# Kernel optimization log

Measured on AMD Instinct MI355X. Metric: run time of the kernel, lower is better.

The kernel has to match this reference:

```python
import jax, jax.numpy as jnp
import numpy as np

DIM = 1024
H = 16
HD = DIM // H
SCALE = HD ** -0.5
LAMBDA_INIT = 0.1
EPS = 1e-6


def setup_inputs() -> dict:
    key0 = jax.random.key(0)
    ks = jax.random.split(key0, 12)
    B, Nq, Nk = 2, 1024, 2048
    w = 0.02
    inp = {
        "query": jax.random.normal(ks[0], (B, Nq, DIM), jnp.float32),
        "key": jax.random.normal(ks[1], (B, Nk, DIM), jnp.float32),
        "value": jax.random.normal(ks[2], (B, Nk, DIM), jnp.float32),
        "qpos": jax.random.randint(ks[3], (B, Nq), 0, Nq, jnp.int32),
        "kpos": jax.random.randint(ks[4], (B, Nk), 0, Nk, jnp.int32),
        "q1_w": jax.random.normal(ks[5], (DIM, DIM), jnp.float32) * w,
        "q2_w": jax.random.normal(ks[6], (DIM, DIM), jnp.float32) * w,
        "kv1_w": jax.random.normal(ks[7], (2 * DIM, DIM), jnp.float32) * w,
        "kv2_w": jax.random.normal(ks[8], (2 * DIM, DIM), jnp.float32) * w,
        "proj_w": jax.random.normal(ks[9], (DIM, DIM), jnp.float32) * w,
        "proj_b": jnp.zeros((DIM,), jnp.float32),
        "norm_w": jnp.ones((DIM,), jnp.float32),
        "lambda_1": jnp.ones((1, H, 1, 1), jnp.float32),
        # layer_idx=0, max_layer=12 -> scale = 1/12
        "lambda_2": jnp.full((1, H, 1, 1), 1.0 - LAMBDA_INIT * (1.0 / 12.0), jnp.float32),
    }
    return inp


def _split_heads(x, B, N):
    # [B, N, DIM] -> [B, H, N, HD]
    return x.reshape(B, N, H, HD).transpose(0, 2, 1, 3)


def reference(query, key, value, qpos, kpos, q1_w, q2_w, kv1_w, kv2_w,
              proj_w, proj_b, norm_w, lambda_1, lambda_2):
    B, Nq, C = query.shape
    Nk = key.shape[1]

    q1 = _split_heads(query @ q1_w.T, B, Nq)
    q2 = _split_heads(query @ q2_w.T, B, Nq)

    kv1 = (key @ kv1_w.T).reshape(B, Nk, 2, H, HD).transpose(2, 0, 3, 1, 4)
    k1, v1 = kv1[0], kv1[1]  # [B, H, Nk, HD]
    kv2 = (key @ kv2_w.T).reshape(B, Nk, 2, H, HD).transpose(2, 0, 3, 1, 4)
    k2 = kv2[0]

    attn1 = jax.nn.softmax(jnp.einsum('bhqd,bhkd->bhqk', q1, k1) * SCALE, axis=-1)
    attn2 = jax.nn.softmax(jnp.einsum('bhqd,bhkd->bhqk', q2, k2) * SCALE, axis=-1)

    lambda_full = lambda_1 - lambda_2 + LAMBDA_INIT  # [1, H, 1, 1]
    diff_attn = attn1 - lambda_full * attn2

    x = jnp.einsum('bhqk,bhkd->bhqd', diff_attn, v1)
    x = x.transpose(0, 2, 1, 3).reshape(B, Nq, C)

    # RMSNorm (computed in float32 like the original)
    xf = x.astype(jnp.float32)
    xf = xf * jax.lax.rsqrt(jnp.mean(xf * xf, axis=-1, keepdims=True) + EPS) * norm_w
    x = xf.astype(x.dtype)

    return x @ proj_w.T + proj_b
```

## Files before the change

### kernel.cpp

```cpp
#include <hip/hip_runtime.h>
#include <cstdint>

typedef unsigned short u16;
typedef __bf16 bf16x8 __attribute__((ext_vector_type(8)));
typedef float f32x4 __attribute__((ext_vector_type(4)));

#define SCALE_LOG2E (0.125f * 1.44269504088896340736f)

__device__ __forceinline__ u16 f2bf(float f) {
    uint32_t u = __builtin_bit_cast(uint32_t, f);
    u += 0x7fff + ((u >> 16) & 1);
    return (u16)(u >> 16);
}
__device__ __forceinline__ float bf2f(u16 u) {
    return __builtin_bit_cast(float, (uint32_t)u << 16);
}

__device__ __forceinline__ void gload_lds16(const void* g, void* l) {
    __builtin_amdgcn_global_load_lds(
        (__attribute__((address_space(1))) void*)g,
        (__attribute__((address_space(3))) void*)l, 16, 0, 0);
}

__global__ __launch_bounds__(256) void cvt_all(const float* __restrict__ s0,
                                               const float* __restrict__ s1,
                                               const float* __restrict__ s2,
                                               const float* __restrict__ s3,
                                               const float* __restrict__ s4,
                                               const float* __restrict__ s5,
                                               const float* __restrict__ s6,
                                               u16* __restrict__ d0, u16* __restrict__ d1,
                                               u16* __restrict__ d2, u16* __restrict__ d3,
                                               u16* __restrict__ d4) {
    int i = blockIdx.x * 256 + threadIdx.x;
    const float* src;
    u16* dst;
    int off;
    if (i < 524288)       { src = s0; dst = d0; off = i; }
    else if (i < 1572864) { src = s1; dst = d1; off = i - 524288; }
    else if (i < 1835008) { src = s2; dst = d2; off = i - 1572864; }
    else if (i < 2097152) { src = s3; dst = d2 + (size_t)1024 * 1024; off = i - 1835008; }
    else if (i < 2621440) { src = s4; dst = d3; off = i - 2097152; }
    else if (i < 2883584) { src = s5; dst = d3 + (size_t)2048 * 1024; off = i - 2621440; }
    else                  { src = s6; dst = d4; off = i - 2883584; }
    float4 v = ((const float4*)src)[off];
    ushort4 o;
    o.x = f2bf(v.x); o.y = f2bf(v.y); o.z = f2bf(v.z); o.w = f2bf(v.w);
    ((ushort4*)dst)[off] = o;
}

__global__ __launch_bounds__(256) void gemm_qkv(const u16* __restrict__ Xq,
                                                const u16* __restrict__ Wq,
                                                const u16* __restrict__ Xk,
                                                const u16* __restrict__ Wkv,
                                                u16* __restrict__ q1s, u16* __restrict__ q2s,
                                                u16* __restrict__ k1s, u16* __restrict__ v1t,
                                                u16* __restrict__ k2s) {
    __shared__ u16 As[128 * 32];
    __shared__ u16 Bs[128 * 32];
    const int K = 1024;
    const int bid = blockIdx.x;
    int mode, bm, bn;
    const u16 *A, *B;
    if (bid < 256) {
        mode = 0; bm = bid >> 4; bn = bid & 15; A = Xq; B = Wq;
    } else {
        int t = bid - 256;
        mode = 1; bm = t / 24; bn = t % 24; A = Xk; B = Wkv;
    }
    const int tid = threadIdx.x;
    const int l = tid & 63, w = tid >> 6;
    const int c = l & 15, g = l >> 4;
    const int wr = w >> 1, wc = w & 1;

    f32x4 acc[4][4];
#pragma unroll
    for (int i = 0; i < 4; i++)
#pragma unroll
        for (int j = 0; j < 4; j++) acc[i][j] = f32x4{0.f, 0.f, 0.f, 0.f};

    const u16* Abase = A + (size_t)(bm * 128) * K;
    const u16* Bbase = B + (size_t)(bn * 128) * K;
    const int r0 = 32 * w + (l >> 2);
    const int ch = (l & 3) * 8;

    for (int kb = 0; kb < K; kb += 32) {
        gload_lds16(Abase + (size_t)r0 * K + kb + ch,        As + 32 * w * 32);
        gload_lds16(Abase + (size_t)(r0 + 16) * K + kb + ch, As + (32 * w + 16) * 32);
        gload_lds16(Bbase + (size_t)r0 * K + kb + ch,        Bs + 32 * w * 32);
        gload_lds16(Bbase + (size_t)(r0 + 16) * K + kb + ch, Bs + (32 * w + 16) * 32);
        __syncthreads();
        bf16x8 af[4], bfr[4];
#pragma unroll
        for (int mi = 0; mi < 4; mi++)
            af[mi] = *(const bf16x8*)&As[(64 * wr + 16 * mi + c) * 32 + 8 * g];
#pragma unroll
        for (int ni = 0; ni < 4; ni++)
            bfr[ni] = *(const bf16x8*)&Bs[(64 * wc + 16 * ni + c) * 32 + 8 * g];
#pragma unroll
        for (int mi = 0; mi < 4; mi++)
#pragma unroll
            for (int ni = 0; ni < 4; ni++)
                acc[mi][ni] = __builtin_amdgcn_mfma_f32_16x16x32_bf16(
                    af[mi], bfr[ni], acc[mi][ni], 0, 0, 0);
        __syncthreads();
    }

#pragma unroll
    for (int mi = 0; mi < 4; mi++)
#pragma unroll
        for (int ni = 0; ni < 4; ni++)
#pragma unroll
            for (int j = 0; j < 4; j++) {
                int m = bm * 128 + 64 * wr + 16 * mi + 4 * g + j;
                int n = bn * 128 + 64 * wc + 16 * ni + c;
                float v = acc[mi][ni][j];
                if (mode == 0) {
                    int b = m >> 10, nq = m & 1023;
                    int half = n >> 10, nn = n & 1023;
                    int h = nn >> 6, hd = nn & 63;
                    u16* dst = half ? q2s : q1s;
                    dst[(size_t)((b * 16 + h) * 1024 + nq) * 64 + hd] = f2bf(v * SCALE_LOG2E);
                } else {
                    int b = m >> 11, nk = m & 2047;
                    if (n < 1024) {
                        int h = n >> 6, hd = n & 63;
                        k1s[(size_t)((b * 16 + h) * 2048 + nk) * 64 + hd] = f2bf(v);
                    } else if (n < 2048) {
                        int nn = n - 1024, h = nn >> 6, hd = nn & 63;
                        v1t[(size_t)((b * 16 + h) * 64 + hd) * 2048 + nk] = f2bf(v);
                    } else {
                        int nn = n - 2048, h = nn >> 6, hd = nn & 63;
                        k2s[(size_t)((b * 16 + h) * 2048 + nk) * 64 + hd] = f2bf(v);
                    }
                }
            }
}

__global__ __launch_bounds__(256) void gemm_proj(const u16* __restrict__ A,
                                                 const u16* __restrict__ B,
                                                 float* __restrict__ fo,
                                                 const float* __restrict__ bias) {
    __shared__ u16 As[128 * 32];
    __shared__ u16 Bs[64 * 32];
    const int K = 1024;
    const int bm = blockIdx.x >> 4, bn = blockIdx.x & 15;
    const int tid = threadIdx.x;
    const int l = tid & 63, w = tid >> 6;
    const int c = l & 15, g = l >> 4;
    const int wr = w >> 1, wc = w & 1;

    f32x4 acc[4][2];
#pragma unroll
    for (int i = 0; i < 4; i++)
#pragma unroll
        for (int j = 0; j < 2; j++) acc[i][j] = f32x4{0.f, 0.f, 0.f, 0.f};

    const u16* Abase = A + (size_t)(bm * 128) * K;
    const u16* Bbase = B + (size_t)(bn * 64) * K;
    const int rA = 32 * w + (l >> 2);
    const int rB = 16 * w + (l >> 2);
    const int ch = (l & 3) * 8;

    for (int kb = 0; kb < K; kb += 32) {
        gload_lds16(Abase + (size_t)rA * K + kb + ch,        As + 32 * w * 32);
        gload_lds16(Abase + (size_t)(rA + 16) * K + kb + ch, As + (32 * w + 16) * 32);
        gload_lds16(Bbase + (size_t)rB * K + kb + ch,        Bs + 16 * w * 32);
        __syncthreads();
        bf16x8 af[4], bfr[2];
#pragma unroll
        for (int mi = 0; mi < 4; mi++)
            af[mi] = *(const bf16x8*)&As[(64 * wr + 16 * mi + c) * 32 + 8 * g];
#pragma unroll
        for (int ni = 0; ni < 2; ni++)
            bfr[ni] = *(const bf16x8*)&Bs[(32 * wc + 16 * ni + c) * 32 + 8 * g];
#pragma unroll
        for (int mi = 0; mi < 4; mi++)
#pragma unroll
            for (int ni = 0; ni < 2; ni++)
                acc[mi][ni] = __builtin_amdgcn_mfma_f32_16x16x32_bf16(
                    af[mi], bfr[ni], acc[mi][ni], 0, 0, 0);
        __syncthreads();
    }

#pragma unroll
    for (int mi = 0; mi < 4; mi++)
#pragma unroll
        for (int ni = 0; ni < 2; ni++)
#pragma unroll
            for (int j = 0; j < 4; j++) {
                int m = bm * 128 + 64 * wr + 16 * mi + 4 * g + j;
                int n = bn * 64 + 32 * wc + 16 * ni + c;
                fo[(size_t)m * 1024 + n] = acc[mi][ni][j] + bias[n];
            }
}

__global__ __launch_bounds__(256) void attn_kernel(const u16* __restrict__ q1s,
                                                   const u16* __restrict__ q2s,
                                                   const u16* __restrict__ k1s,
                                                   const u16* __restrict__ k2s,
                                                   const u16* __restrict__ v1t,
                                                   u16* __restrict__ Opart,
                                                   float* __restrict__ Lpart) {
    __shared__ __bf16 P1[4][32 * 72];
    __shared__ __bf16 P2[4][32 * 72];
    const int tid = threadIdx.x;
    const int l = tid & 63, w = tid >> 6;
    const int c = l & 15, g = l >> 4;
    const int bid = blockIdx.x;
    const int xcd = bid & 7, slot = bid >> 3;
    const int bh = xcd * 4 + (slot >> 5);
    const int r = slot & 31;
    const int qt = r >> 2, s = r & 3;
    const int b = bh >> 4, h = bh & 15;
    const int q0 = qt * 128 + w * 32;

    bf16x8 qf1[2][2], qf2[2][2];
#pragma unroll
    for (int qq = 0; qq < 2; qq++) {
        const u16* p1 = q1s + (size_t)(bh * 1024 + q0 + qq * 16 + c) * 64 + 8 * g;
        const u16* p2 = q2s + (size_t)(bh * 1024 + q0 + qq * 16 + c) * 64 + 8 * g;
        qf1[qq][0] = *(const bf16x8*)p1; qf1[qq][1] = *(const bf16x8*)(p1 + 32);
        qf2[qq][0] = *(const bf16x8*)p2; qf2[qq][1] = *(const bf16x8*)(p2 + 32);
    }

    f32x4 O1[2][4], O2[2][4], la1[2], la2[2];
#pragma unroll
    for (int qq = 0; qq < 2; qq++) {
        la1[qq] = la2[qq] = f32x4{0.f, 0.f, 0.f, 0.f};
#pragma unroll
        for (int dt = 0; dt < 4; dt++) O1[qq][dt] = O2[qq][dt] = f32x4{0.f, 0.f, 0.f, 0.f};
    }

    const u16* k1b = k1s + (size_t)bh * 2048 * 64;
    const u16* k2b = k2s + (size_t)bh * 2048 * 64;
    const u16* vb  = v1t + (size_t)bh * 64 * 2048;
    __bf16* Pb1 = &P1[w][0];
    __bf16* Pb2 = &P2[w][0];

    const int kb0 = s * 512;
    for (int it = 0; it < 8; it++) {
        const int kb = kb0 + it * 64;
        bf16x8 k1f[4][2];
#pragma unroll
        for (int kt = 0; kt < 4; kt++) {
            const u16* p = k1b + (size_t)(kb + kt * 16 + c) * 64 + 8 * g;
            k1f[kt][0] = *(const bf16x8*)p; k1f[kt][1] = *(const bf16x8*)(p + 32);
        }
        bf16x8 vf[4][2];
#pragma unroll
        for (int dt = 0; dt < 4; dt++) {
            const u16* pv = vb + (size_t)(dt * 16 + c) * 2048 + kb + 8 * g;
            vf[dt][0] = *(const bf16x8*)pv; vf[dt][1] = *(const bf16x8*)(pv + 32);
        }
#pragma unroll
        for (int qq = 0; qq < 2; qq++)
#pragma unroll
            for (int kt = 0; kt < 4; kt++) {
                f32x4 z = f32x4{0.f, 0.f, 0.f, 0.f};
                z = __builtin_amdgcn_mfma_f32_16x16x32_bf16(qf1[qq][0], k1f[kt][0], z, 0, 0, 0);
                z = __builtin_amdgcn_mfma_f32_16x16x32_bf16(qf1[qq][1], k1f[kt][1], z, 0, 0, 0);
#pragma unroll
                for (int j = 0; j < 4; j++) {
                    float p = __builtin_exp2f(z[j]);
                    la1[qq][j] += p;
                    Pb1[(qq * 16 + 4 * g + j) * 72 + kt * 16 + c] = (__bf16)p;
                }
            }
        bf16x8 k2f[4][2];
#pragma unroll
        for (int kt = 0; kt < 4; kt++) {
            const u16* p = k2b + (size_t)(kb + kt * 16 + c) * 64 + 8 * g;
            k2f[kt][0] = *(const bf16x8*)p; k2f[kt][1] = *(const bf16x8*)(p + 32);
        }
#pragma unroll
        for (int qq = 0; qq < 2; qq++)
#pragma unroll
            for (int kt = 0; kt < 4; kt++) {
                f32x4 z = f32x4{0.f, 0.f, 0.f, 0.f};
                z = __builtin_amdgcn_mfma_f32_16x16x32_bf16(qf2[qq][0], k2f[kt][0], z, 0, 0, 0);
                z = __builtin_amdgcn_mfma_f32_16x16x32_bf16(qf2[qq][1], k2f[kt][1], z, 0, 0, 0);
#pragma unroll
                for (int j = 0; j < 4; j++) {
                    float p = __builtin_exp2f(z[j]);
                    la2[qq][j] += p;
                    Pb2[(qq * 16 + 4 * g + j) * 72 + kt * 16 + c] = (__bf16)p;
                }
            }
        bf16x8 pa1[2][2], pa2[2][2];
#pragma unroll
        for (int qq = 0; qq < 2; qq++)
#pragma unroll
            for (int ks = 0; ks < 2; ks++) {
                pa1[qq][ks] = *(const bf16x8*)&Pb1[(qq * 16 + c) * 72 + ks * 32 + 8 * g];
                pa2[qq][ks] = *(const bf16x8*)&Pb2[(qq * 16 + c) * 72 + ks * 32 + 8 * g];
            }
#pragma unroll
        for (int qq = 0; qq < 2; qq++)
#pragma unroll
            for (int dt = 0; dt < 4; dt++) {
                O1[qq][dt] = __builtin_amdgcn_mfma_f32_16x16x32_bf16(pa1[qq][0], vf[dt][0], O1[qq][dt], 0, 0, 0);
                O1[qq][dt] = __builtin_amdgcn_mfma_f32_16x16x32_bf16(pa1[qq][1], vf[dt][1], O1[qq][dt], 0, 0, 0);
                O2[qq][dt] = __builtin_amdgcn_mfma_f32_16x16x32_bf16(pa2[qq][0], vf[dt][0], O2[qq][dt], 0, 0, 0);
                O2[qq][dt] = __builtin_amdgcn_mfma_f32_16x16x32_bf16(pa2[qq][1], vf[dt][1], O2[qq][dt], 0, 0, 0);
            }
    }

#pragma unroll
    for (int off = 1; off < 16; off <<= 1)
#pragma unroll
        for (int qq = 0; qq < 2; qq++)
#pragma unroll
            for (int j = 0; j < 4; j++) {
                la1[qq][j] += __shfl_xor(la1[qq][j], off, 64);
                la2[qq][j] += __shfl_xor(la2[qq][j], off, 64);
            }

#pragma unroll
    for (int qq = 0; qq < 2; qq++)
#pragma unroll
        for (int dt = 0; dt < 4; dt++)
#pragma unroll
            for (int j = 0; j < 4; j++) {
                size_t rowg = (size_t)b * 1024 + q0 + qq * 16 + 4 * g + j;
                size_t col = h * 64 + dt * 16 + c;
                Opart[((size_t)(s * 2 + 0) * 2048 + rowg) * 1024 + col] = f2bf(O1[qq][dt][j]);
                Opart[((size_t)(s * 2 + 1) * 2048 + rowg) * 1024 + col] = f2bf(O2[qq][dt][j]);
            }
    if (c == 0) {
#pragma unroll
        for (int qq = 0; qq < 2; qq++)
#pragma unroll
            for (int j = 0; j < 4; j++) {
                size_t rowg = (size_t)b * 1024 + q0 + qq * 16 + 4 * g + j;
                Lpart[((size_t)(s * 2 + 0) * 2048 + rowg) * 16 + h] = la1[qq][j];
                Lpart[((size_t)(s * 2 + 1) * 2048 + rowg) * 16 + h] = la2[qq][j];
            }
    }
}

__global__ __launch_bounds__(256) void combine_rms(const u16* __restrict__ Opart,
                                                   const float* __restrict__ Lpart,
                                                   const float* __restrict__ lam1,
                                                   const float* __restrict__ lam2,
                                                   const float* __restrict__ nw,
                                                   u16* __restrict__ xn) {
    const int row = blockIdx.x, t = threadIdx.x;
    const int h = t >> 4;
    float a1[4] = {0.f, 0.f, 0.f, 0.f}, a2[4] = {0.f, 0.f, 0.f, 0.f};
    float li1 = 0.f, li2 = 0.f;
#pragma unroll
    for (int s = 0; s < 4; s++) {
        ushort4 u1 = ((const ushort4*)(Opart + ((size_t)(s * 2 + 0) * 2048 + row) * 1024))[t];
        ushort4 u2 = ((const ushort4*)(Opart + ((size_t)(s * 2 + 1) * 2048 + row) * 1024))[t];
        a1[0] += bf2f(u1.x); a1[1] += bf2f(u1.y); a1[2] += bf2f(u1.z); a1[3] += bf2f(u1.w);
        a2[0] += bf2f(u2.x); a2[1] += bf2f(u2.y); a2[2] += bf2f(u2.z); a2[3] += bf2f(u2.w);
        li1 += Lpart[((size_t)(s * 2 + 0) * 2048 + row) * 16 + h];
        li2 += Lpart[((size_t)(s * 2 + 1) * 2048 + row) * 16 + h];
    }
    float lam = lam1[h] - lam2[h] + 0.1f;
    float i1 = 1.0f / li1, i2 = lam / li2;
    float x0 = a1[0] * i1 - a2[0] * i2;
    float x1 = a1[1] * i1 - a2[1] * i2;
    float x2 = a1[2] * i1 - a2[2] * i2;
    float x3 = a1[3] * i1 - a2[3] * i2;
    float ss = x0 * x0 + x1 * x1 + x2 * x2 + x3 * x3;
#pragma unroll
    for (int off = 1; off < 64; off <<= 1) ss += __shfl_xor(ss, off, 64);
    __shared__ float ws4[4];
    if ((t & 63) == 0) ws4[t >> 6] = ss;
    __syncthreads();
    float tot = ws4[0] + ws4[1] + ws4[2] + ws4[3];
    float rs = rsqrtf(tot * (1.0f / 1024.0f) + 1e-6f);
    float4 wv = ((const float4*)nw)[t];
    ushort4 o;
    o.x = f2bf(x0 * rs * wv.x);
    o.y = f2bf(x1 * rs * wv.y);
    o.z = f2bf(x2 * rs * wv.z);
    o.w = f2bf(x3 * rs * wv.w);
    ((ushort4*)(xn + (size_t)row * 1024))[t] = o;
}

extern "C" void kernel_launch(void* const* d_in, const int* in_sizes, int n_in,
                              void* d_out, int out_size, void* d_ws, size_t ws_size,
                              hipStream_t stream) {
    const float* query  = (const float*)d_in[0];
    const float* key    = (const float*)d_in[1];
    const float* q1_w   = (const float*)d_in[5];
    const float* q2_w   = (const float*)d_in[6];
    const float* kv1_w  = (const float*)d_in[7];
    const float* kv2_w  = (const float*)d_in[8];
    const float* proj_w = (const float*)d_in[9];
    const float* proj_b = (const float*)d_in[10];
    const float* norm_w = (const float*)d_in[11];
    const float* lam1   = (const float*)d_in[12];
    const float* lam2   = (const float*)d_in[13];
    float* out = (float*)d_out;

    char* ws = (char*)d_ws;
    size_t off = 0;
    auto alloc = [&](size_t bytes) {
        void* p = ws + off;
        off += (bytes + 255) & ~(size_t)255;
        return p;
    };
    u16* Xq   = (u16*)alloc((size_t)2048 * 1024 * 2);
    u16* Xk   = (u16*)alloc((size_t)4096 * 1024 * 2);
    u16* Wq   = (u16*)alloc((size_t)2048 * 1024 * 2);
    u16* Wkv  = (u16*)alloc((size_t)3072 * 1024 * 2);
    u16* Wp   = (u16*)alloc((size_t)1024 * 1024 * 2);
    u16* q1sb = (u16*)alloc((size_t)32 * 1024 * 64 * 2);
    u16* q2sb = (u16*)alloc((size_t)32 * 1024 * 64 * 2);
    u16* k1sb = (u16*)alloc((size_t)32 * 2048 * 64 * 2);
    u16* k2sb = (u16*)alloc((size_t)32 * 2048 * 64 * 2);
    u16* v1tb = (u16*)alloc((size_t)32 * 64 * 2048 * 2);
    u16* Opart = (u16*)alloc((size_t)8 * 2048 * 1024 * 2);
    float* Lpart = (float*)alloc((size_t)8 * 2048 * 16 * 4);
    u16* xn   = (u16*)alloc((size_t)2048 * 1024 * 2);

    cvt_all<<<12288, 256, 0, stream>>>(query, key, q1_w, q2_w, kv1_w, kv2_w, proj_w,
                                       Xq, Xk, Wq, Wkv, Wp);

    gemm_qkv<<<1024, 256, 0, stream>>>(Xq, Wq, Xk, Wkv, q1sb, q2sb, k1sb, v1tb, k2sb);

    attn_kernel<<<1024, 256, 0, stream>>>(q1sb, q2sb, k1sb, k2sb, v1tb, Opart, Lpart);

    combine_rms<<<2048, 256, 0, stream>>>(Opart, Lpart, lam1, lam2, norm_w, xn);

    gemm_proj<<<256, 256, 0, stream>>>(xn, Wp, out, proj_b);
}
```

Baseline: 307.0 us.

## Compute transposed S with 32x32 MFMA and keep P in registers via permlane swap

The attention kernel is rewritten to compute S^T = K·Q^T with 32x32x16 bf16 MFMAs, so each lane owns one query column. The exponentiated P values are packed with v_cvt_pk_bf16_f32 and rearranged with v_permlane32_swap into the A-operand layout for the PV MFMA. This removes the per-wave LDS round trip for P and the 16-lane shuffle reduction of row sums. The trade-offs are larger accumulator tiles, which raise register pressure, more key-loop iterations over smaller key tiles, and a dependence on gfx950-specific inline assembly.

After: 303.6 us. Within noise of the previous version (-1.1%).

```diff
diff --git a/kernel.cpp b/kernel.cpp
--- a/kernel.cpp
+++ b/kernel.cpp
@@ -4,6 +4,8 @@
 typedef unsigned short u16;
 typedef __bf16 bf16x8 __attribute__((ext_vector_type(8)));
 typedef float f32x4 __attribute__((ext_vector_type(4)));
+typedef float f32x16 __attribute__((ext_vector_type(16)));
+typedef uint32_t u32x4 __attribute__((ext_vector_type(4)));
 
 #define SCALE_LOG2E (0.125f * 1.44269504088896340736f)
 
@@ -202,140 +204,140 @@
                                                    const u16* __restrict__ v1t,
                                                    u16* __restrict__ Opart,
                                                    float* __restrict__ Lpart) {
-    __shared__ __bf16 P1[4][32 * 72];
-    __shared__ __bf16 P2[4][32 * 72];
     const int tid = threadIdx.x;
     const int l = tid & 63, w = tid >> 6;
-    const int c = l & 15, g = l >> 4;
+    const int c5 = l & 31, hf = l >> 5;
     const int bid = blockIdx.x;
     const int xcd = bid & 7, slot = bid >> 3;
     const int bh = xcd * 4 + (slot >> 5);
     const int r = slot & 31;
     const int qt = r >> 2, s = r & 3;
-    const int b = bh >> 4, h = bh & 15;
+    const int b = bh >> 4, head = bh & 15;
     const int q0 = qt * 128 + w * 32;
 
-    bf16x8 qf1[2][2], qf2[2][2];
-#pragma unroll
-    for (int qq = 0; qq < 2; qq++) {
-        const u16* p1 = q1s + (size_t)(bh * 1024 + q0 + qq * 16 + c) * 64 + 8 * g;
-        const u16* p2 = q2s + (size_t)(bh * 1024 + q0 + qq * 16 + c) * 64 + 8 * g;
-        qf1[qq][0] = *(const bf16x8*)p1; qf1[qq][1] = *(const bf16x8*)(p1 + 32);
-        qf2[qq][0] = *(const bf16x8*)p2; qf2[qq][1] = *(const bf16x8*)(p2 + 32);
-    }
-
-    f32x4 O1[2][4], O2[2][4], la1[2], la2[2];
-#pragma unroll
-    for (int qq = 0; qq < 2; qq++) {
-        la1[qq] = la2[qq] = f32x4{0.f, 0.f, 0.f, 0.f};
-#pragma unroll
-        for (int dt = 0; dt < 4; dt++) O1[qq][dt] = O2[qq][dt] = f32x4{0.f, 0.f, 0.f, 0.f};
-    }
-
-    const u16* k1b = k1s + (size_t)bh * 2048 * 64;
-    const u16* k2b = k2s + (size_t)bh * 2048 * 64;
-    const u16* vb  = v1t + (size_t)bh * 64 * 2048;
-    __bf16* Pb1 = &P1[w][0];
-    __bf16* Pb2 = &P2[w][0];
+    bf16x8 qB1[4], qB2[4];
+    {
+        const u16* p1 = q1s + (size_t)(bh * 1024 + q0 + c5) * 64 + 8 * hf;
+        const u16* p2 = q2s + (size_t)(bh * 1024 + q0 + c5) * 64 + 8 * hf;
+#pragma unroll
+        for (int d = 0; d < 4; d++) {
+            qB1[d] = *(const bf16x8*)(p1 + 16 * d);
+            qB2[d] = *(const bf16x8*)(p2 + 16 * d);
+        }
+    }
+
+    f32x16 O1[2], O2[2];
+#pragma unroll
+    for (int dh = 0; dh < 2; dh++)
+#pragma unroll
+        for (int i = 0; i < 16; i++) { O1[dh][i] = 0.f; O2[dh][i] = 0.f; }
+    float la1 = 0.f, la2 = 0.f;
+
+    const u16* k1b = k1s + (size_t)bh * 2048 * 64 + 8 * hf;
+    const u16* k2b = k2s + (size_t)bh * 2048 * 64 + 8 * hf;
+    const u16* vb  = v1t + (size_t)bh * 64 * 2048 + 8 * hf;
 
     const int kb0 = s * 512;
-    for (int it = 0; it < 8; it++) {
-        const int kb = kb0 + it * 64;
-        bf16x8 k1f[4][2];
-#pragma unroll
-        for (int kt = 0; kt < 4; kt++) {
-            const u16* p = k1b + (size_t)(kb + kt * 16 + c) * 64 + 8 * g;
-            k1f[kt][0] = *(const bf16x8*)p; k1f[kt][1] = *(const bf16x8*)(p + 32);
+    for (int it = 0; it < 16; it++) {
+        const int kb = kb0 + it * 32;
+        bf16x8 kA1[4], kA2[4];
+        {
+            const u16* p1 = k1b + (size_t)(kb + c5) * 64;
+            const u16* p2 = k2b + (size_t)(kb + c5) * 64;
+#pragma unroll
+            for (int d = 0; d < 4; d++) {
+                kA1[d] = *(const bf16x8*)(p1 + 16 * d);
+                kA2[d] = *(const bf16x8*)(p2 + 16 * d);
+            }
         }
-        bf16x8 vf[4][2];
-#pragma unroll
-        for (int dt = 0; dt < 4; dt++) {
-            const u16* pv = vb + (size_t)(dt * 16 + c) * 2048 + kb + 8 * g;
-            vf[dt][0] = *(const bf16x8*)pv; vf[dt][1] = *(const bf16x8*)(pv + 32);
+        bf16x8 vB[2][2];
+#pragma unroll
+        for (int dh = 0; dh < 2; dh++)
+#pragma unroll
+            for (int kk = 0; kk < 2; kk++)
+                vB[dh][kk] = *(const bf16x8*)(vb + (size_t)(dh * 32 + c5) * 2048 + kb + kk * 16);
+
+        {
+            f32x16 S;
+#pragma unroll
+            for (int i = 0; i < 16; i++) S[i] = 0.f;
+#pragma unroll
+            for (int d = 0; d < 4; d++)
+                S = __builtin_amdgcn_mfma_f32_32x32x16_bf16(kA1[d], qB1[d], S, 0, 0, 0);
+            uint32_t dpk[8];
+#pragma unroll
+            for (int i = 0; i < 8; i++) {
+                float pa = __builtin_exp2f(S[2 * i]);
+                float pb = __builtin_exp2f(S[2 * i + 1]);
+                la1 += pa + pb;
+                asm("v_cvt_pk_bf16_f32 %0, %1, %2" : "=v"(dpk[i]) : "v"(pa), "v"(pb));
+            }
+            uint32_t a0 = dpk[0], b0 = dpk[2], a1 = dpk[1], b1 = dpk[3];
+            asm("v_permlane32_swap_b32 %0, %1" : "+v"(a0), "+v"(b0));
+            asm("v_permlane32_swap_b32 %0, %1" : "+v"(a1), "+v"(b1));
+            u32x4 t0 = {a0, a1, b0, b1};
+            bf16x8 pf0 = __builtin_bit_cast(bf16x8, t0);
+            uint32_t a2 = dpk[4], b2 = dpk[6], a3 = dpk[5], b3 = dpk[7];
+            asm("v_permlane32_swap_b32 %0, %1" : "+v"(a2), "+v"(b2));
+            asm("v_permlane32_swap_b32 %0, %1" : "+v"(a3), "+v"(b3));
+            u32x4 t1 = {a2, a3, b2, b3};
+            bf16x8 pf1 = __builtin_bit_cast(bf16x8, t1);
+#pragma unroll
+            for (int dh = 0; dh < 2; dh++) {
+                O1[dh] = __builtin_amdgcn_mfma_f32_32x32x16_bf16(pf0, vB[dh][0], O1[dh], 0, 0, 0);
+                O1[dh] = __builtin_amdgcn_mfma_f32_32x32x16_bf16(pf1, vB[dh][1], O1[dh], 0, 0, 0);
+            }
         }
-#pragma unroll
-        for (int qq = 0; qq < 2; qq++)
-#pragma unroll
-            for (int kt = 0; kt < 4; kt++) {
-                f32x4 z = f32x4{0.f, 0.f, 0.f, 0.f};
-                z = __builtin_amdgcn_mfma_f32_16x16x32_bf16(qf1[qq][0], k1f[kt][0], z, 0, 0, 0);
-                z = __builtin_amdgcn_mfma_f32_16x16x32_bf16(qf1[qq][1], k1f[kt][1], z, 0, 0, 0);
-#pragma unroll
-                for (int j = 0; j < 4; j++) {
-                    float p = __builtin_exp2f(z[j]);
-                    la1[qq][j] += p;
-                    Pb1[(qq * 16 + 4 * g + j) * 72 + kt * 16 + c] = (__bf16)p;
-                }
-            }
-        bf16x8 k2f[4][2];
-#pragma unroll
-        for (int kt = 0; kt < 4; kt++) {
-            const u16* p = k2b + (size_t)(kb + kt * 16 + c) * 64 + 8 * g;
-            k2f[kt][0] = *(const bf16x8*)p; k2f[kt][1] = *(const bf16x8*)(p + 32);
+        {
+            f32x16 S;
+#pragma unroll
+            for (int i = 0; i < 16; i++) S[i] = 0.f;
+#pragma unroll
+            for (int d = 0; d < 4; d++)
+                S = __builtin_amdgcn_mfma_f32_32x32x16_bf16(kA2[d], qB2[d], S, 0, 0, 0);
+            uint32_t dpk[8];
+#pragma unroll
+            for (int i = 0; i < 8; i++) {
+                float pa = __builtin_exp2f(S[2 * i]);
+                float pb = __builtin_exp2f(S[2 * i + 1]);
+                la2 += pa + pb;
+                asm("v_cvt_pk_bf16_f32 %0, %1, %2" : "=v"(dpk[i]) : "v"(pa), "v"(pb));
+            }
+            uint32_t a0 = dpk[0], b0 = dpk[2], a1 = dpk[1], b1 = dpk[3];
+            asm("v_permlane32_swap_b32 %0, %1" : "+v"(a0), "+v"(b0));
+            asm("v_permlane32_swap_b32 %0, %1" : "+v"(a1), "+v"(b1));
+            u32x4 t0 = {a0, a1, b0, b1};
+            bf16x8 pf0 = __builtin_bit_cast(bf16x8, t0);
+            uint32_t a2 = dpk[4], b2 = dpk[6], a3 = dpk[5], b3 = dpk[7];
+            asm("v_permlane32_swap_b32 %0, %1" : "+v"(a2), "+v"(b2));
+            asm("v_permlane32_swap_b32 %0, %1" : "+v"(a3), "+v"(b3));
+            u32x4 t1 = {a2, a3, b2, b3};
+            bf16x8 pf1 = __builtin_bit_cast(bf16x8, t1);
+#pragma unroll
+            for (int dh = 0; dh < 2; dh++) {
+                O2[dh] = __builtin_amdgcn_mfma_f32_32x32x16_bf16(pf0, vB[dh][0], O2[dh], 0, 0, 0);
+                O2[dh] = __builtin_amdgcn_mfma_f32_32x32x16_bf16(pf1, vB[dh][1], O2[dh], 0, 0, 0);
+            }
         }
-#pragma unroll
-        for (int qq = 0; qq < 2; qq++)
-#pragma unroll
-            for (int kt = 0; kt < 4; kt++) {
-                f32x4 z = f32x4{0.f, 0.f, 0.f, 0.f};
-                z = __builtin_amdgcn_mfma_f32_16x16x32_bf16(qf2[qq][0], k2f[kt][0], z, 0, 0, 0);
-                z = __builtin_amdgcn_mfma_f32_16x16x32_bf16(qf2[qq][1], k2f[kt][1], z, 0, 0, 0);
-#pragma unroll
-                for (int j = 0; j < 4; j++) {
-                    float p = __builtin_exp2f(z[j]);
-                    la2[qq][j] += p;
-                    Pb2[(qq * 16 + 4 * g + j) * 72 + kt * 16 + c] = (__bf16)p;
-                }
-            }
-        bf16x8 pa1[2][2], pa2[2][2];
-#pragma unroll
-        for (int qq = 0; qq < 2; qq++)
-#pragma unroll
-            for (int ks = 0; ks < 2; ks++) {
-                pa1[qq][ks] = *(const bf16x8*)&Pb1[(qq * 16 + c) * 72 + ks * 32 + 8 * g];
-                pa2[qq][ks] = *(const bf16x8*)&Pb2[(qq * 16 + c) * 72 + ks * 32 + 8 * g];
-            }
-#pragma unroll
-        for (int qq = 0; qq < 2; qq++)
-#pragma unroll
-            for (int dt = 0; dt < 4; dt++) {
-                O1[qq][dt] = __builtin_amdgcn_mfma_f32_16x16x32_bf16(pa1[qq][0], vf[dt][0], O1[qq][dt], 0, 0, 0);
-                O1[qq][dt] = __builtin_amdgcn_mfma_f32_16x16x32_bf16(pa1[qq][1], vf[dt][1], O1[qq][dt], 0, 0, 0);
-                O2[qq][dt] = __builtin_amdgcn_mfma_f32_16x16x32_bf16(pa2[qq][0], vf[dt][0], O2[qq][dt], 0, 0, 0);
-                O2[qq][dt] = __builtin_amdgcn_mfma_f32_16x16x32_bf16(pa2[qq][1], vf[dt][1], O2[qq][dt], 0, 0, 0);
-            }
-    }
-
-#pragma unroll
-    for (int off = 1; off < 16; off <<= 1)
-#pragma unroll
-        for (int qq = 0; qq < 2; qq++)
-#pragma unroll
-            for (int j = 0; j < 4; j++) {
-                la1[qq][j] += __shfl_xor(la1[qq][j], off, 64);
-                la2[qq][j] += __shfl_xor(la2[qq][j], off, 64);
-            }
-
-#pragma unroll
-    for (int qq = 0; qq < 2; qq++)
-#pragma unroll
-        for (int dt = 0; dt < 4; dt++)
-#pragma unroll
-            for (int j = 0; j < 4; j++) {
-                size_t rowg = (size_t)b * 1024 + q0 + qq * 16 + 4 * g + j;
-                size_t col = h * 64 + dt * 16 + c;
-                Opart[((size_t)(s * 2 + 0) * 2048 + rowg) * 1024 + col] = f2bf(O1[qq][dt][j]);
-                Opart[((size_t)(s * 2 + 1) * 2048 + rowg) * 1024 + col] = f2bf(O2[qq][dt][j]);
-            }
-    if (c == 0) {
-#pragma unroll
-        for (int qq = 0; qq < 2; qq++)
-#pragma unroll
-            for (int j = 0; j < 4; j++) {
-                size_t rowg = (size_t)b * 1024 + q0 + qq * 16 + 4 * g + j;
-                Lpart[((size_t)(s * 2 + 0) * 2048 + rowg) * 16 + h] = la1[qq][j];
-                Lpart[((size_t)(s * 2 + 1) * 2048 + rowg) * 16 + h] = la2[qq][j];
-            }
+    }
+
+    la1 += __shfl_xor(la1, 32, 64);
+    la2 += __shfl_xor(la2, 32, 64);
+
+#pragma unroll
+    for (int dh = 0; dh < 2; dh++)
+#pragma unroll
+        for (int rr = 0; rr < 16; rr++) {
+            int qrow = (rr & 3) + 8 * (rr >> 2) + 4 * hf;
+            size_t rowg = (size_t)b * 1024 + q0 + qrow;
+            size_t col = head * 64 + dh * 32 + c5;
+            Opart[((size_t)(s * 2 + 0) * 2048 + rowg) * 1024 + col] = f2bf(O1[dh][rr]);
+            Opart[((size_t)(s * 2 + 1) * 2048 + rowg) * 1024 + col] = f2bf(O2[dh][rr]);
+        }
+    if (hf == 0) {
+        size_t rowg = (size_t)b * 1024 + q0 + c5;
+        Lpart[((size_t)(s * 2 + 0) * 2048 + rowg) * 16 + head] = la1;
+        Lpart[((size_t)(s * 2 + 1) * 2048 + rowg) * 16 + head] = la2;
     }
 }
 
```
